# Performance work log

Hardware: AMD Instinct MI355X
Metric: run time of the kernel (lower is better)

The kernel has to match this reference:

```python
import jax, jax.numpy as jnp
import numpy as np

D_MODEL = 1024
NHEAD = 16
HEAD_DIM = D_MODEL // NHEAD


def setup_inputs() -> dict:
    key = jax.random.key(0)
    ks = jax.random.split(key, 9)
    s = 0.02
    x = jax.random.normal(ks[0], (2, 2048, D_MODEL), dtype=jnp.float32)
    Wq = jax.random.normal(ks[1], (D_MODEL, D_MODEL), dtype=jnp.float32) * s
    bq = jnp.zeros((D_MODEL,), jnp.float32)
    Wk = jax.random.normal(ks[2], (D_MODEL, D_MODEL), dtype=jnp.float32) * s
    bk = jnp.zeros((D_MODEL,), jnp.float32)
    Wv = jax.random.normal(ks[3], (D_MODEL, D_MODEL), dtype=jnp.float32) * s
    bv = jnp.zeros((D_MODEL,), jnp.float32)
    Wo = jax.random.normal(ks[4], (D_MODEL, D_MODEL), dtype=jnp.float32) * s
    bo = jnp.zeros((D_MODEL,), jnp.float32)
    return {"x": x, "Wq": Wq, "bq": bq, "Wk": Wk, "bk": bk,
            "Wv": Wv, "bv": bv, "Wo": Wo, "bo": bo}


def _rope(x, sin, cos):
    # x: [B, L, H, Dh]; rotate-half as in the torch module
    half = x.shape[-1] // 2
    x1, x2 = x[..., :half], x[..., half:]
    rotated = jnp.concatenate([-x2, x1], axis=-1)
    return x * cos + rotated * sin


def reference(x, Wq, bq, Wk, bk, Wv, bv, Wo, bo):
    B, L, D = x.shape
    H, Dh = NHEAD, HEAD_DIM
    q = (x @ Wq.T + bq).reshape(B, L, H, Dh)
    k = (x @ Wk.T + bk).reshape(B, L, H, Dh)
    v = (x @ Wv.T + bv).reshape(B, L, H, Dh)

    inv_freq = 1.0 / (10000.0 ** (jnp.arange(0, Dh, 2, dtype=jnp.float32) / Dh))
    t = jnp.arange(L, dtype=jnp.float32)
    freqs = jnp.einsum('i,j->ij', t, inv_freq)          # [L, Dh/2]
    emb = jnp.concatenate([freqs, freqs], axis=-1)      # [L, Dh]
    cos = jnp.cos(emb)[None, :, None, :]
    sin = jnp.sin(emb)[None, :, None, :]

    q = _rope(q, sin, cos)
    k = _rope(k, sin, cos)

    # [B, H, L, L]
    scores = jnp.einsum('bqhd,bkhd->bhqk', q, k) / jnp.sqrt(jnp.float32(Dh))
    attn = jax.nn.softmax(scores, axis=-1)
    # dropout in eval mode = identity (p given as 0.0)
    out = jnp.einsum('bhqk,bkhd->bqhd', attn, v).reshape(B, L, D)
    return out @ Wo.T + bo
```

## Files before the change

kernel.cpp:

```cpp
#include <hip/hip_runtime.h>
#include <math.h>

#define D_MODEL 1024
#define NHEAD 16
#define HEAD_DIM 64
#define L_SEQ 2048
#define BATCH 2
#define M_ROWS 4096
#define SC_Q 0.18033688011112042f

typedef __attribute__((ext_vector_type(8))) short short8;
typedef __attribute__((ext_vector_type(4))) float floatx4;

#if __has_builtin(__builtin_amdgcn_exp2f)
#define EXP2F(x) __builtin_amdgcn_exp2f(x)
#else
#define EXP2F(x) exp2f(x)
#endif

__device__ inline unsigned f2bf_u(float x) {
    unsigned u = __float_as_uint(x);
    return (u + 0x7fffu + ((u >> 16) & 1u)) >> 16;
}

__device__ inline void gl_lds16(const void* g, void* l) {
    __builtin_amdgcn_global_load_lds((const __attribute__((address_space(1))) void*)g,
                                     (__attribute__((address_space(3))) void*)l, 16, 0, 0);
}

__global__ __launch_bounds__(256) void cvt_all(
    const float* __restrict__ x,  const float* __restrict__ wq,
    const float* __restrict__ wk, const float* __restrict__ wv,
    const float* __restrict__ wo,
    unsigned short* __restrict__ xb,  unsigned short* __restrict__ wqb,
    unsigned short* __restrict__ wkb, unsigned short* __restrict__ wvb,
    unsigned short* __restrict__ wob, float* __restrict__ rt) {
    if (blockIdx.y == 5) {
        for (int idx = blockIdx.x * 256 + threadIdx.x; idx < L_SEQ * 16;
             idx += gridDim.x * 256) {
            int l = idx >> 4, f = idx & 15;
            float if0 = (float)pow(10000.0, -(double)f / 32.0);
            float if1 = (float)pow(10000.0, -(double)(f + 16) / 32.0);
            float s0, c0, s1, c1;
            sincosf((float)l * if0, &s0, &c0);
            sincosf((float)l * if1, &s1, &c1);
            float4 v = {c0, c1, s0, s1};
            *(float4*)(rt + (size_t)idx * 4) = v;
        }
        return;
    }
    const float* s; unsigned short* d; int n;
    switch (blockIdx.y) {
        case 0:  s = x;  d = xb;  n = M_ROWS * D_MODEL; break;
        case 1:  s = wq; d = wqb; n = D_MODEL * D_MODEL; break;
        case 2:  s = wk; d = wkb; n = D_MODEL * D_MODEL; break;
        case 3:  s = wv; d = wvb; n = D_MODEL * D_MODEL; break;
        default: s = wo; d = wob; n = D_MODEL * D_MODEL; break;
    }
    int stride = gridDim.x * 256 * 4;
    for (int i = (blockIdx.x * 256 + threadIdx.x) * 4; i < n; i += stride) {
        float4 v = *(const float4*)(s + i);
        ushort4 o;
        o.x = (unsigned short)f2bf_u(v.x);
        o.y = (unsigned short)f2bf_u(v.y);
        o.z = (unsigned short)f2bf_u(v.z);
        o.w = (unsigned short)f2bf_u(v.w);
        *(ushort4*)(d + i) = o;
    }
}

__global__ __launch_bounds__(256) void gemm_qkv(
    const unsigned short* __restrict__ xb,
    const unsigned short* __restrict__ wqb, const unsigned short* __restrict__ wkb,
    const unsigned short* __restrict__ wvb,
    const float* __restrict__ bq, const float* __restrict__ bk,
    const float* __restrict__ bv, const float* __restrict__ rt,
    unsigned short* __restrict__ qo, unsigned short* __restrict__ ko,
    unsigned short* __restrict__ vo) {
    __shared__ __align__(16) unsigned short As[128 * 32];
    __shared__ __align__(16) unsigned short Bs[128 * 32];

    const int K = D_MODEL;
    const int tid = threadIdx.x;
    const int lane = tid & 63;
    const int w = tid >> 6;
    const int wm = (w & 1) * 64;
    const int wn = (w >> 1) * 64;
    const int m0 = blockIdx.x * 128;
    const int n0 = blockIdx.y * 128;

    const unsigned short* Wsel; const float* bsel;
    unsigned short* osel; int mode; float oscale;
    if (blockIdx.z == 0)      { Wsel = wqb; bsel = bq; osel = qo; mode = 1; oscale = SC_Q; }
    else if (blockIdx.z == 1) { Wsel = wkb; bsel = bk; osel = ko; mode = 1; oscale = 1.0f; }
    else                      { Wsel = wvb; bsel = bv; osel = vo; mode = 2; oscale = 1.0f; }

    floatx4 acc[4][4];
#pragma unroll
    for (int i = 0; i < 4; ++i)
#pragma unroll
        for (int j = 0; j < 4; ++j) acc[i][j] = (floatx4){0.f, 0.f, 0.f, 0.f};

    const int sr = lane >> 2;
    const int ss = lane & 3;
    const unsigned short* Ag = xb + (size_t)m0 * K;
    const unsigned short* Bg = Wsel + (size_t)n0 * K;

    for (int k0 = 0; k0 < K; k0 += 32) {
        __syncthreads();
#pragma unroll
        for (int t = 0; t < 2; ++t) {
            int R0 = t * 64 + w * 16;
            int r = R0 + sr;
            int c = ss ^ ((r >> 1) & 3);
            gl_lds16(Ag + (size_t)r * K + k0 + c * 8, (void*)(As + R0 * 32));
            gl_lds16(Bg + (size_t)r * K + k0 + c * 8, (void*)(Bs + R0 * 32));
        }
        __syncthreads();

        short8 af[4], bf[4];
#pragma unroll
        for (int mt = 0; mt < 4; ++mt) {
            int ar = wm + mt * 16 + (lane & 15);
            int slot = (lane >> 4) ^ ((ar >> 1) & 3);
            af[mt] = *(const short8*)(As + ar * 32 + slot * 8);
        }
#pragma unroll
        for (int nt = 0; nt < 4; ++nt) {
            int br = wn + nt * 16 + (lane & 15);
            int slot = (lane >> 4) ^ ((br >> 1) & 3);
            bf[nt] = *(const short8*)(Bs + br * 32 + slot * 8);
        }
#pragma unroll
        for (int mt = 0; mt < 4; ++mt)
#pragma unroll
            for (int nt = 0; nt < 4; ++nt)
                acc[mt][nt] = __builtin_amdgcn_mfma_f32_16x16x32_bf16(
                    af[mt], bf[nt], acc[mt][nt], 0, 0, 0);
    }

#pragma unroll
    for (int nt = 0; nt < 4; ++nt) {
        float bn = bsel[n0 + wn + nt * 16 + (lane & 15)];
#pragma unroll
        for (int mt = 0; mt < 4; ++mt)
#pragma unroll
            for (int i = 0; i < 4; ++i) acc[mt][nt][i] += bn;
    }

    const int h = (n0 + wn) >> 6;

    if (mode == 1) {
#pragma unroll
        for (int mt = 0; mt < 4; ++mt)
#pragma unroll
            for (int i = 0; i < 4; ++i) {
                int m = m0 + wm + mt * 16 + (lane >> 4) * 4 + i;
                int b = m >> 11, l = m & (L_SEQ - 1);
                float4 tc = *(const float4*)(rt + ((size_t)(l * 16 + (lane & 15)) << 2));
#pragma unroll
                for (int nt = 0; nt < 4; ++nt) {
                    int dh = nt * 16 + (lane & 15);
                    float partner = acc[mt][nt ^ 2][i];
                    float rot = (nt < 2) ? -partner : partner;
                    float c = (nt & 1) ? tc.y : tc.x;
                    float s = (nt & 1) ? tc.w : tc.z;
                    float val = (acc[mt][nt][i] * c + rot * s) * oscale;
                    size_t idx = (((size_t)(b * NHEAD + h)) * L_SEQ + l) * HEAD_DIM + dh;
                    osel[idx] = (unsigned short)f2bf_u(val);
                }
            }
    } else {
#pragma unroll
        for (int mt = 0; mt < 4; ++mt)
#pragma unroll
            for (int ih = 0; ih < 4; ih += 2) {
                int m = m0 + wm + mt * 16 + (lane >> 4) * 4 + ih;
                int b = m >> 11, l = m & (L_SEQ - 1);
#pragma unroll
                for (int nt = 0; nt < 4; ++nt) {
                    int dh = nt * 16 + (lane & 15);
                    unsigned v0 = f2bf_u(acc[mt][nt][ih]);
                    unsigned v1 = f2bf_u(acc[mt][nt][ih + 1]);
                    size_t idx = (((size_t)(b * NHEAD + h)) * HEAD_DIM + dh) * L_SEQ + l;
                    *(unsigned*)(vo + idx) = v0 | (v1 << 16);
                }
            }
    }
}

__global__ __launch_bounds__(256) void gemm_out(
    const unsigned short* __restrict__ A, const unsigned short* __restrict__ Wb,
    const float* __restrict__ bias, float* __restrict__ out) {
    __shared__ __align__(16) unsigned short As[64 * 32];
    __shared__ __align__(16) unsigned short Bs[128 * 32];

    const int K = D_MODEL;
    const int tid = threadIdx.x;
    const int lane = tid & 63;
    const int w = tid >> 6;
    const int wm = (w & 1) * 32;
    const int wn = (w >> 1) * 64;
    const int m0 = blockIdx.x * 64;
    const int n0 = blockIdx.y * 128;

    floatx4 acc[2][4];
#pragma unroll
    for (int i = 0; i < 2; ++i)
#pragma unroll
        for (int j = 0; j < 4; ++j) acc[i][j] = (floatx4){0.f, 0.f, 0.f, 0.f};

    const int sr = lane >> 2;
    const int ss = lane & 3;
    const unsigned short* Ag = A + (size_t)m0 * K;
    const unsigned short* Bg = Wb + (size_t)n0 * K;

    for (int k0 = 0; k0 < K; k0 += 32) {
        __syncthreads();
        {
            int r = w * 16 + sr;
            int c = ss ^ ((r >> 1) & 3);
            gl_lds16(Ag + (size_t)r * K + k0 + c * 8, (void*)(As + (w * 16) * 32));
        }
#pragma unroll
        for (int t = 0; t < 2; ++t) {
            int R0 = t * 64 + w * 16;
            int r = R0 + sr;
            int c = ss ^ ((r >> 1) & 3);
            gl_lds16(Bg + (size_t)r * K + k0 + c * 8, (void*)(Bs + R0 * 32));
        }
        __syncthreads();

        short8 af[2], bf[4];
#pragma unroll
        for (int mt = 0; mt < 2; ++mt) {
            int ar = wm + mt * 16 + (lane & 15);
            int slot = (lane >> 4) ^ ((ar >> 1) & 3);
            af[mt] = *(const short8*)(As + ar * 32 + slot * 8);
        }
#pragma unroll
        for (int nt = 0; nt < 4; ++nt) {
            int br = wn + nt * 16 + (lane & 15);
            int slot = (lane >> 4) ^ ((br >> 1) & 3);
            bf[nt] = *(const short8*)(Bs + br * 32 + slot * 8);
        }
#pragma unroll
        for (int mt = 0; mt < 2; ++mt)
#pragma unroll
            for (int nt = 0; nt < 4; ++nt)
                acc[mt][nt] = __builtin_amdgcn_mfma_f32_16x16x32_bf16(
                    af[mt], bf[nt], acc[mt][nt], 0, 0, 0);
    }

#pragma unroll
    for (int nt = 0; nt < 4; ++nt) {
        int n = n0 + wn + nt * 16 + (lane & 15);
        float bn = bias[n];
#pragma unroll
        for (int mt = 0; mt < 2; ++mt)
#pragma unroll
            for (int i = 0; i < 4; ++i) {
                int m = m0 + wm + mt * 16 + (lane >> 4) * 4 + i;
                out[(size_t)m * D_MODEL + n] = acc[mt][nt][i] + bn;
            }
    }
}

template <int NZ>
__global__ __launch_bounds__(256, 4) void attn_mfma(
    const unsigned short* __restrict__ q, const unsigned short* __restrict__ k,
    const unsigned short* __restrict__ vt,
    float* __restrict__ opart, float* __restrict__ lpart,
    unsigned short* __restrict__ ao) {
    __shared__ __align__(16) unsigned short Ks[64 * 64];
    __shared__ __align__(16) unsigned short Vs[64 * 64];
    __shared__ __align__(16) unsigned short Ps[4 * 32 * 72];

    const int tid = threadIdx.x;
    const int lane = tid & 63;
    const int w = tid >> 6;
    const int bh = blockIdx.y;
    const int q0 = blockIdx.x * 128;
    const int z = blockIdx.z;
    const int kvbase = z * (L_SEQ / NZ);

    const unsigned short* qb = q + (size_t)bh * L_SEQ * HEAD_DIM;
    const unsigned short* kb = k + (size_t)bh * L_SEQ * HEAD_DIM;
    const unsigned short* vb = vt + (size_t)bh * HEAD_DIM * L_SEQ;

    short8 qf[2][2];
#pragma unroll
    for (int mt = 0; mt < 2; ++mt)
#pragma unroll
        for (int ks = 0; ks < 2; ++ks)
            qf[mt][ks] = *(const short8*)(
                qb + (size_t)(q0 + w * 32 + mt * 16 + (lane & 15)) * HEAD_DIM
                + ks * 32 + (lane >> 4) * 8);

    floatx4 o[2][4];
    floatx4 ls[2];
#pragma unroll
    for (int mt = 0; mt < 2; ++mt) {
        ls[mt] = (floatx4){0.f, 0.f, 0.f, 0.f};
#pragma unroll
        for (int j = 0; j < 4; ++j) o[mt][j] = (floatx4){0.f, 0.f, 0.f, 0.f};
    }

    short8 ones;
#pragma unroll
    for (int j = 0; j < 8; ++j) ones[j] = (short)0x3F80;

    unsigned short* Psw = Ps + w * (32 * 72);
    const int sr = lane >> 3;
    const int ss = lane & 7;

    for (int t = 0; t < L_SEQ / (64 * NZ); ++t) {
        int kv0 = kvbase + t * 64;
        __syncthreads();
#pragma unroll
        for (int tt = 0; tt < 2; ++tt) {
            int R0 = tt * 32 + w * 8;
            int r = R0 + sr;
            int c = ss ^ (r & 7);
            gl_lds16(kb + (size_t)(kv0 + r) * HEAD_DIM + c * 8, (void*)(Ks + R0 * 64));
            gl_lds16(vb + (size_t)r * L_SEQ + kv0 + c * 8, (void*)(Vs + R0 * 64));
        }
        __syncthreads();

        floatx4 s[2][4];
#pragma unroll
        for (int mt = 0; mt < 2; ++mt)
#pragma unroll
            for (int nt = 0; nt < 4; ++nt) s[mt][nt] = (floatx4){0.f, 0.f, 0.f, 0.f};
#pragma unroll
        for (int ks = 0; ks < 2; ++ks)
#pragma unroll
            for (int nt = 0; nt < 4; ++nt) {
                int br = nt * 16 + (lane & 15);
                int slot = (ks * 4 + (lane >> 4)) ^ (br & 7);
                short8 bfr = *(const short8*)(Ks + br * 64 + slot * 8);
                s[0][nt] = __builtin_amdgcn_mfma_f32_16x16x32_bf16(qf[0][ks], bfr, s[0][nt], 0, 0, 0);
                s[1][nt] = __builtin_amdgcn_mfma_f32_16x16x32_bf16(qf[1][ks], bfr, s[1][nt], 0, 0, 0);
            }

#pragma unroll
        for (int mt = 0; mt < 2; ++mt)
#pragma unroll
            for (int i = 0; i < 4; ++i) {
                int row = mt * 16 + (lane >> 4) * 4 + i;
#pragma unroll
                for (int nt = 0; nt < 4; ++nt) {
                    float p = EXP2F(s[mt][nt][i]);
                    Psw[row * 72 + nt * 16 + (lane & 15)] =
                        (unsigned short)(__float_as_uint(p) >> 16);
                }
            }

#pragma unroll
        for (int ks = 0; ks < 2; ++ks) {
            short8 a0 = *(const short8*)(Psw + (lane & 15) * 72 + (ks * 4 + (lane >> 4)) * 8);
            short8 a1 = *(const short8*)(Psw + (16 + (lane & 15)) * 72 + (ks * 4 + (lane >> 4)) * 8);
            ls[0] = __builtin_amdgcn_mfma_f32_16x16x32_bf16(a0, ones, ls[0], 0, 0, 0);
            ls[1] = __builtin_amdgcn_mfma_f32_16x16x32_bf16(a1, ones, ls[1], 0, 0, 0);
#pragma unroll
            for (int nt = 0; nt < 4; ++nt) {
                int br = nt * 16 + (lane & 15);
                int slot = (ks * 4 + (lane >> 4)) ^ (br & 7);
                short8 bfr = *(const short8*)(Vs + br * 64 + slot * 8);
                o[0][nt] = __builtin_amdgcn_mfma_f32_16x16x32_bf16(a0, bfr, o[0][nt], 0, 0, 0);
                o[1][nt] = __builtin_amdgcn_mfma_f32_16x16x32_bf16(a1, bfr, o[1][nt], 0, 0, 0);
            }
        }
    }

    if (NZ == 1) {
        const int b = bh >> 4, h = bh & (NHEAD - 1);
#pragma unroll
        for (int mt = 0; mt < 2; ++mt)
#pragma unroll
            for (int i = 0; i < 4; ++i) {
                int l = q0 + w * 32 + mt * 16 + (lane >> 4) * 4 + i;
                float inv = 1.0f / ls[mt][i];
#pragma unroll
                for (int nt = 0; nt < 4; ++nt) {
                    int dh = nt * 16 + (lane & 15);
                    size_t idx = ((size_t)b * L_SEQ + l) * D_MODEL + h * HEAD_DIM + dh;
                    ao[idx] = (unsigned short)f2bf_u(o[mt][nt][i] * inv);
                }
            }
    } else {
        const size_t base = ((size_t)z * (BATCH * NHEAD) + bh) * L_SEQ;
#pragma unroll
        for (int mt = 0; mt < 2; ++mt)
#pragma unroll
            for (int i = 0; i < 4; ++i) {
                int l = q0 + w * 32 + mt * 16 + (lane >> 4) * 4 + i;
#pragma unroll
                for (int nt = 0; nt < 4; ++nt) {
                    int dh = nt * 16 + (lane & 15);
                    opart[(base + l) * HEAD_DIM + dh] = o[mt][nt][i];
                }
            }
        if ((lane & 15) == 0) {
#pragma unroll
            for (int mt = 0; mt < 2; ++mt)
#pragma unroll
                for (int i = 0; i < 4; ++i) {
                    int l = q0 + w * 32 + mt * 16 + (lane >> 4) * 4 + i;
                    lpart[base + l] = ls[mt][i];
                }
        }
    }
}

__global__ __launch_bounds__(256) void attn_combine(
    const float* __restrict__ opart, const float* __restrict__ lpart,
    unsigned short* __restrict__ ao) {
    const size_t R = (size_t)BATCH * NHEAD * L_SEQ;
    int e = blockIdx.x * 256 + threadIdx.x;
    int r = e >> 4;
    int dh0 = (e & 15) * 4;
    float4 a = *(const float4*)(opart + (size_t)r * HEAD_DIM + dh0);
    float4 c = *(const float4*)(opart + (R + r) * HEAD_DIM + dh0);
    float inv = 1.0f / (lpart[r] + lpart[R + r]);
    int bh = r >> 11, l = r & (L_SEQ - 1);
    int b = bh >> 4, h = bh & (NHEAD - 1);
    ushort4 ov;
    ov.x = (unsigned short)f2bf_u((a.x + c.x) * inv);
    ov.y = (unsigned short)f2bf_u((a.y + c.y) * inv);
    ov.z = (unsigned short)f2bf_u((a.z + c.z) * inv);
    ov.w = (unsigned short)f2bf_u((a.w + c.w) * inv);
    *(ushort4*)(ao + ((size_t)b * L_SEQ + l) * D_MODEL + h * HEAD_DIM + dh0) = ov;
}

extern "C" void kernel_launch(void* const* d_in, const int* in_sizes, int n_in,
                              void* d_out, int out_size, void* d_ws, size_t ws_size,
                              hipStream_t stream) {
    const float* x  = (const float*)d_in[0];
    const float* Wq = (const float*)d_in[1];
    const float* bq = (const float*)d_in[2];
    const float* Wk = (const float*)d_in[3];
    const float* bk = (const float*)d_in[4];
    const float* Wv = (const float*)d_in[5];
    const float* bv = (const float*)d_in[6];
    const float* Wo = (const float*)d_in[7];
    const float* bo = (const float*)d_in[8];
    float* outp = (float*)d_out;

    const size_t XE = (size_t)M_ROWS * D_MODEL;
    const size_t WE = (size_t)D_MODEL * D_MODEL;
    unsigned short* wqb = (unsigned short*)d_ws;
    unsigned short* wkb = wqb + WE;
    unsigned short* wvb = wkb + WE;
    unsigned short* wob = wvb + WE;
    unsigned short* qbf = wob + WE;
    unsigned short* kbf = qbf + XE;
    unsigned short* vtb = kbf + XE;
    unsigned short* xb  = vtb + XE;
    unsigned short* aob = xb;
    float* rt    = (float*)(xb + XE);
    float* lpart = rt;
    float* opart = rt + 131072;

    const size_t base_bytes  = (4 * WE + 4 * XE) * 2 + 131072 * 4;
    const size_t split_bytes = base_bytes + (size_t)8 * 1024 * 1024 * 4;
    const bool use_split = ws_size >= split_bytes;

    cvt_all<<<dim3(1024, 6), 256, 0, stream>>>(x, Wq, Wk, Wv, Wo,
                                               xb, wqb, wkb, wvb, wob, rt);

    gemm_qkv<<<dim3(M_ROWS / 128, D_MODEL / 128, 3), 256, 0, stream>>>(
        xb, wqb, wkb, wvb, bq, bk, bv, rt, qbf, kbf, vtb);

    if (use_split) {
        attn_mfma<2><<<dim3(L_SEQ / 128, BATCH * NHEAD, 2), 256, 0, stream>>>(
            qbf, kbf, vtb, opart, lpart, nullptr);
        attn_combine<<<dim3(4096), 256, 0, stream>>>(opart, lpart, aob);
    } else {
        attn_mfma<1><<<dim3(L_SEQ / 128, BATCH * NHEAD, 1), 256, 0, stream>>>(
            qbf, kbf, vtb, nullptr, nullptr, aob);
    }

    gemm_out<<<dim3(M_ROWS / 64, D_MODEL / 128), 256, 0, stream>>>(aob, wob, bo, outp);
}
```

Measured before the change: 196.3 us.

## Compute transposed scores so P stays in registers as fp16 MFMA operand

The attention inner loop now computes S^T = K·Q^T, so each lane's accumulator output already matches the A-operand layout of a 16x16x16 fp16 MFMA. Exponentials are packed straight into fp16 registers and fed to the PV and row-sum MFMAs, which removes the per-wave LDS round trip for P and its shared buffer. V is now stored as fp16 (pkrtz) instead of bf16 to match. This trades the K=32 bf16 MFMAs for twice as many K=16 fp16 ones, and fp16 P or V values could overflow or lose range if scores grow large.

```diff
diff --git a/kernel.cpp b/kernel.cpp
--- a/kernel.cpp
+++ b/kernel.cpp
@@ -11,6 +11,8 @@
 
 typedef __attribute__((ext_vector_type(8))) short short8;
 typedef __attribute__((ext_vector_type(4))) float floatx4;
+typedef __attribute__((ext_vector_type(2))) __fp16 half2_t;
+typedef __attribute__((ext_vector_type(4))) __fp16 half4_t;
 
 #if __has_builtin(__builtin_amdgcn_exp2f)
 #define EXP2F(x) __builtin_amdgcn_exp2f(x)
@@ -180,10 +182,10 @@
 #pragma unroll
                 for (int nt = 0; nt < 4; ++nt) {
                     int dh = nt * 16 + (lane & 15);
-                    unsigned v0 = f2bf_u(acc[mt][nt][ih]);
-                    unsigned v1 = f2bf_u(acc[mt][nt][ih + 1]);
+                    union { half2_t h; unsigned u; } cv;
+                    cv.h = __builtin_amdgcn_cvt_pkrtz(acc[mt][nt][ih], acc[mt][nt][ih + 1]);
                     size_t idx = (((size_t)(b * NHEAD + h)) * HEAD_DIM + dh) * L_SEQ + l;
-                    *(unsigned*)(vo + idx) = v0 | (v1 << 16);
+                    *(unsigned*)(vo + idx) = cv.u;
                 }
             }
     }
@@ -274,11 +276,12 @@
     unsigned short* __restrict__ ao) {
     __shared__ __align__(16) unsigned short Ks[64 * 64];
     __shared__ __align__(16) unsigned short Vs[64 * 64];
-    __shared__ __align__(16) unsigned short Ps[4 * 32 * 72];
 
     const int tid = threadIdx.x;
     const int lane = tid & 63;
     const int w = tid >> 6;
+    const int quad = lane >> 4;
+    const int ln = lane & 15;
     const int bh = blockIdx.y;
     const int q0 = blockIdx.x * 128;
     const int z = blockIdx.z;
@@ -290,27 +293,26 @@
 
     short8 qf[2][2];
 #pragma unroll
-    for (int mt = 0; mt < 2; ++mt)
+    for (int ntq = 0; ntq < 2; ++ntq)
 #pragma unroll
         for (int ks = 0; ks < 2; ++ks)
-            qf[mt][ks] = *(const short8*)(
-                qb + (size_t)(q0 + w * 32 + mt * 16 + (lane & 15)) * HEAD_DIM
-                + ks * 32 + (lane >> 4) * 8);
+            qf[ntq][ks] = *(const short8*)(
+                qb + (size_t)(q0 + w * 32 + ntq * 16 + ln) * HEAD_DIM
+                + ks * 32 + quad * 8);
 
     floatx4 o[2][4];
     floatx4 ls[2];
 #pragma unroll
-    for (int mt = 0; mt < 2; ++mt) {
-        ls[mt] = (floatx4){0.f, 0.f, 0.f, 0.f};
-#pragma unroll
-        for (int j = 0; j < 4; ++j) o[mt][j] = (floatx4){0.f, 0.f, 0.f, 0.f};
-    }
-
-    short8 ones;
-#pragma unroll
-    for (int j = 0; j < 8; ++j) ones[j] = (short)0x3F80;
-
-    unsigned short* Psw = Ps + w * (32 * 72);
+    for (int ntq = 0; ntq < 2; ++ntq) {
+        ls[ntq] = (floatx4){0.f, 0.f, 0.f, 0.f};
+#pragma unroll
+        for (int j = 0; j < 4; ++j) o[ntq][j] = (floatx4){0.f, 0.f, 0.f, 0.f};
+    }
+
+    half4_t ones;
+#pragma unroll
+    for (int j = 0; j < 4; ++j) ones[j] = (__fp16)1.0f;
+
     const int sr = lane >> 3;
     const int ss = lane & 7;
 
@@ -327,48 +329,44 @@
         }
         __syncthreads();
 
-        floatx4 s[2][4];
-#pragma unroll
-        for (int mt = 0; mt < 2; ++mt)
-#pragma unroll
-            for (int nt = 0; nt < 4; ++nt) s[mt][nt] = (floatx4){0.f, 0.f, 0.f, 0.f};
-#pragma unroll
-        for (int ks = 0; ks < 2; ++ks)
-#pragma unroll
-            for (int nt = 0; nt < 4; ++nt) {
-                int br = nt * 16 + (lane & 15);
-                int slot = (ks * 4 + (lane >> 4)) ^ (br & 7);
-                short8 bfr = *(const short8*)(Ks + br * 64 + slot * 8);
-                s[0][nt] = __builtin_amdgcn_mfma_f32_16x16x32_bf16(qf[0][ks], bfr, s[0][nt], 0, 0, 0);
-                s[1][nt] = __builtin_amdgcn_mfma_f32_16x16x32_bf16(qf[1][ks], bfr, s[1][nt], 0, 0, 0);
-            }
-
-#pragma unroll
-        for (int mt = 0; mt < 2; ++mt)
-#pragma unroll
-            for (int i = 0; i < 4; ++i) {
-                int row = mt * 16 + (lane >> 4) * 4 + i;
-#pragma unroll
-                for (int nt = 0; nt < 4; ++nt) {
-                    float p = EXP2F(s[mt][nt][i]);
-                    Psw[row * 72 + nt * 16 + (lane & 15)] =
-                        (unsigned short)(__float_as_uint(p) >> 16);
-                }
-            }
-
-#pragma unroll
-        for (int ks = 0; ks < 2; ++ks) {
-            short8 a0 = *(const short8*)(Psw + (lane & 15) * 72 + (ks * 4 + (lane >> 4)) * 8);
-            short8 a1 = *(const short8*)(Psw + (16 + (lane & 15)) * 72 + (ks * 4 + (lane >> 4)) * 8);
-            ls[0] = __builtin_amdgcn_mfma_f32_16x16x32_bf16(a0, ones, ls[0], 0, 0, 0);
-            ls[1] = __builtin_amdgcn_mfma_f32_16x16x32_bf16(a1, ones, ls[1], 0, 0, 0);
-#pragma unroll
-            for (int nt = 0; nt < 4; ++nt) {
-                int br = nt * 16 + (lane & 15);
-                int slot = (ks * 4 + (lane >> 4)) ^ (br & 7);
-                short8 bfr = *(const short8*)(Vs + br * 64 + slot * 8);
-                o[0][nt] = __builtin_amdgcn_mfma_f32_16x16x32_bf16(a0, bfr, o[0][nt], 0, 0, 0);
-                o[1][nt] = __builtin_amdgcn_mfma_f32_16x16x32_bf16(a1, bfr, o[1][nt], 0, 0, 0);
+#pragma unroll
+        for (int mt = 0; mt < 4; ++mt) {
+            int ar = mt * 16 + ln;
+            short8 kf0 = *(const short8*)(Ks + ar * 64 + ((quad) ^ (ar & 7)) * 8);
+            short8 kf1 = *(const short8*)(Ks + ar * 64 + ((4 + quad) ^ (ar & 7)) * 8);
+
+            floatx4 s0 = (floatx4){0.f, 0.f, 0.f, 0.f};
+            floatx4 s1 = (floatx4){0.f, 0.f, 0.f, 0.f};
+            s0 = __builtin_amdgcn_mfma_f32_16x16x32_bf16(kf0, qf[0][0], s0, 0, 0, 0);
+            s0 = __builtin_amdgcn_mfma_f32_16x16x32_bf16(kf1, qf[0][1], s0, 0, 0, 0);
+            s1 = __builtin_amdgcn_mfma_f32_16x16x32_bf16(kf0, qf[1][0], s1, 0, 0, 0);
+            s1 = __builtin_amdgcn_mfma_f32_16x16x32_bf16(kf1, qf[1][1], s1, 0, 0, 0);
+
+            half4_t vf[4];
+#pragma unroll
+            for (int ntd = 0; ntd < 4; ++ntd) {
+                int row = ntd * 16 + ln;
+                int slot = (mt * 2 + (quad >> 1)) ^ (row & 7);
+                vf[ntd] = *(const half4_t*)(Vs + row * 64 + slot * 8 + (quad & 1) * 4);
+            }
+
+            {
+                half2_t lo = __builtin_amdgcn_cvt_pkrtz(EXP2F(s0[0]), EXP2F(s0[1]));
+                half2_t hi = __builtin_amdgcn_cvt_pkrtz(EXP2F(s0[2]), EXP2F(s0[3]));
+                half4_t af; af.lo = lo; af.hi = hi;
+                ls[0] = __builtin_amdgcn_mfma_f32_16x16x16f16(af, ones, ls[0], 0, 0, 0);
+#pragma unroll
+                for (int ntd = 0; ntd < 4; ++ntd)
+                    o[0][ntd] = __builtin_amdgcn_mfma_f32_16x16x16f16(af, vf[ntd], o[0][ntd], 0, 0, 0);
+            }
+            {
+                half2_t lo = __builtin_amdgcn_cvt_pkrtz(EXP2F(s1[0]), EXP2F(s1[1]));
+                half2_t hi = __builtin_amdgcn_cvt_pkrtz(EXP2F(s1[2]), EXP2F(s1[3]));
+                half4_t af; af.lo = lo; af.hi = hi;
+                ls[1] = __builtin_amdgcn_mfma_f32_16x16x16f16(af, ones, ls[1], 0, 0, 0);
+#pragma unroll
+                for (int ntd = 0; ntd < 4; ++ntd)
+                    o[1][ntd] = __builtin_amdgcn_mfma_f32_16x16x16f16(af, vf[ntd], o[1][ntd], 0, 0, 0);
             }
         }
     }
@@ -376,38 +374,38 @@
     if (NZ == 1) {
         const int b = bh >> 4, h = bh & (NHEAD - 1);
 #pragma unroll
-        for (int mt = 0; mt < 2; ++mt)
+        for (int ntq = 0; ntq < 2; ++ntq)
 #pragma unroll
             for (int i = 0; i < 4; ++i) {
-                int l = q0 + w * 32 + mt * 16 + (lane >> 4) * 4 + i;
-                float inv = 1.0f / ls[mt][i];
-#pragma unroll
-                for (int nt = 0; nt < 4; ++nt) {
-                    int dh = nt * 16 + (lane & 15);
+                int l = q0 + w * 32 + ntq * 16 + quad * 4 + i;
+                float inv = 1.0f / ls[ntq][i];
+#pragma unroll
+                for (int ntd = 0; ntd < 4; ++ntd) {
+                    int dh = ntd * 16 + ln;
                     size_t idx = ((size_t)b * L_SEQ + l) * D_MODEL + h * HEAD_DIM + dh;
-                    ao[idx] = (unsigned short)f2bf_u(o[mt][nt][i] * inv);
+                    ao[idx] = (unsigned short)f2bf_u(o[ntq][ntd][i] * inv);
                 }
             }
     } else {
         const size_t base = ((size_t)z * (BATCH * NHEAD) + bh) * L_SEQ;
 #pragma unroll
-        for (int mt = 0; mt < 2; ++mt)
+        for (int ntq = 0; ntq < 2; ++ntq)
 #pragma unroll
             for (int i = 0; i < 4; ++i) {
-                int l = q0 + w * 32 + mt * 16 + (lane >> 4) * 4 + i;
-#pragma unroll
-                for (int nt = 0; nt < 4; ++nt) {
-                    int dh = nt * 16 + (lane & 15);
-                    opart[(base + l) * HEAD_DIM + dh] = o[mt][nt][i];
+                int l = q0 + w * 32 + ntq * 16 + quad * 4 + i;
+#pragma unroll
+                for (int ntd = 0; ntd < 4; ++ntd) {
+                    int dh = ntd * 16 + ln;
+                    opart[(base + l) * HEAD_DIM + dh] = o[ntq][ntd][i];
                 }
             }
-        if ((lane & 15) == 0) {
-#pragma unroll
-            for (int mt = 0; mt < 2; ++mt)
+        if (ln == 0) {
+#pragma unroll
+            for (int ntq = 0; ntq < 2; ++ntq)
 #pragma unroll
                 for (int i = 0; i < 4; ++i) {
-                    int l = q0 + w * 32 + mt * 16 + (lane >> 4) * 4 + i;
-                    lpart[base + l] = ls[mt][i];
+                    int l = q0 + w * 32 + ntq * 16 + quad * 4 + i;
+                    lpart[base + l] = ls[ntq][i];
                 }
         }
     }
```

After: 198.5 us. No clear change (+1.1%).
